# Optimization experiments

Measured on AMD Instinct MI355X. Metric: run time of the kernel, lower is better.

## Reference

```python
import jax, jax.numpy as jnp
import numpy as np
from jax import lax

K = 3           # dynamic-filter kernel size
NUM_TYPES = 216 # Qstr*Qcohe*Qangle = 3*3*24
C = 64          # in/out channels
GROUP = 4


def _conv(x, w, groups=1):
    return lax.conv_general_dilated(
        x, w, window_strides=(1, 1), padding='SAME',
        dimension_numbers=('NCHW', 'OIHW', 'NCHW'),
        feature_group_count=groups)


def setup_inputs() -> dict:
    key = jax.random.key(0)
    ks = jax.random.split(key, 7)
    B, H, W = 1, 64, 64
    x = jax.random.normal(ks[0], (B, C, H, W), dtype=jnp.float32)
    buckets = jax.random.randint(ks[1], (B, H, W), 0, NUM_TYPES)
    # body1: grouped 3x3 conv (in=out=64, groups=4 -> in/group=16)
    w1 = jax.random.normal(ks[2], (C, C // GROUP, 3, 3), dtype=jnp.float32) * 0.05
    b1 = jax.random.normal(ks[3], (C,), dtype=jnp.float32) * 0.05
    # filter embedding: one flattened (out, in*K*K + bias) filter per bucket type
    emb = jax.random.normal(ks[4], (NUM_TYPES, C * (C * K * K + 1)), dtype=jnp.float32) * 0.1
    # body2: 1x1 conv
    w2 = jax.random.normal(ks[5], (C, C, 1, 1), dtype=jnp.float32) * 0.05
    b2 = jax.random.normal(ks[6], (C,), dtype=jnp.float32) * 0.05
    return {'x': x, 'buckets': buckets, 'w1': w1, 'b1': b1, 'emb': emb, 'w2': w2, 'b2': b2}


def reference(x, buckets, w1, b1, emb, w2, b2):
    B, Cin, H, W = x.shape
    Cout = w2.shape[0]
    ckk = emb.shape[1] // Cout - 1  # in*K*K
    # body1: grouped conv + ReLU
    h = jax.nn.relu(_conv(x, w1, groups=GROUP) + b1[None, :, None, None])
    # per-pixel bucket-indexed dynamic conv
    patches = lax.conv_general_dilated_patches(
        h, (K, K), (1, 1), 'SAME',
        dimension_numbers=('NCHW', 'OIHW', 'NCHW'))  # [B, Cin*K*K, H, W]
    f = emb[buckets].reshape(B, H, W, Cout, ckk + 1)   # gathered per-pixel filters
    out = jnp.einsum('bchw,bhwoc->bohw', patches, f[..., :-1])
    out = out + jnp.transpose(f[..., -1], (0, 3, 1, 2))  # per-pixel bias
    # body2: ReLU -> 1x1 conv
    out = _conv(jax.nn.relu(out), w2) + b2[None, :, None, None]
    # residual + ReLU
    return jax.nn.relu(out + x)
```

## Files before the change

kernel.cpp:

```cpp
#include <hip/hip_runtime.h>

#define NTYPES 216
#define NPIX   4096
#define KD     576
#define ROWLEN 577
#define NPC    32
#define PSTR   640
#define MAXB   160

typedef __attribute__((ext_vector_type(8))) short short8;
typedef __attribute__((ext_vector_type(4))) float f32x4;
typedef __attribute__((ext_vector_type(4), aligned(4))) float f32x4u;
typedef __attribute__((ext_vector_type(8))) unsigned short u16x8;
typedef __attribute__((ext_vector_type(4))) unsigned short u16x4;
typedef __attribute__((ext_vector_type(2))) unsigned short u16x2;

static __device__ __forceinline__ unsigned short f2bf(float f) {
    unsigned u = __builtin_bit_cast(unsigned, f);
    unsigned r = (u + 0x7FFFu + ((u >> 16) & 1u)) >> 16;
    return (unsigned short)r;
}

__global__ __launch_bounds__(256) void prep_kernel(
        const float* __restrict__ x, const float* __restrict__ w1,
        const float* __restrict__ b1, unsigned short* __restrict__ hbf) {
    int tid = threadIdx.x;
    int flat = blockIdx.x * 256 + tid;
    int x4 = flat & 15;
    int y  = (flat >> 4) & 63;
    int c  = flat >> 10;
    int g  = c >> 4;
    const float* wrow = w1 + c * 144;
    float o0, o1, o2, o3;
    o0 = o1 = o2 = o3 = b1[c];
    #pragma unroll
    for (int ci = 0; ci < 16; ++ci) {
        const float* xp = x + (g * 16 + ci) * 4096;
        #pragma unroll
        for (int dy = 0; dy < 3; ++dy) {
            int yy = y + dy - 1;
            if (yy < 0 || yy > 63) continue;
            const float* row = xp + yy * 64 + x4 * 4;
            f32x4 mm = *(const f32x4*)row;
            float xl = (x4 > 0)  ? row[-1] : 0.f;
            float xr = (x4 < 15) ? row[4]  : 0.f;
            float wa = wrow[ci * 9 + dy * 3 + 0];
            float wb = wrow[ci * 9 + dy * 3 + 1];
            float wc = wrow[ci * 9 + dy * 3 + 2];
            o0 = fmaf(wa, xl,    fmaf(wb, mm[0], fmaf(wc, mm[1], o0)));
            o1 = fmaf(wa, mm[0], fmaf(wb, mm[1], fmaf(wc, mm[2], o1)));
            o2 = fmaf(wa, mm[1], fmaf(wb, mm[2], fmaf(wc, mm[3], o2)));
            o3 = fmaf(wa, mm[2], fmaf(wb, mm[3], fmaf(wc, xr,    o3)));
        }
    }
    int pix0 = y * 64 + x4 * 4;
    hbf[(pix0 + 0) * 64 + c] = f2bf(fmaxf(o0, 0.f));
    hbf[(pix0 + 1) * 64 + c] = f2bf(fmaxf(o1, 0.f));
    hbf[(pix0 + 2) * 64 + c] = f2bf(fmaxf(o2, 0.f));
    hbf[(pix0 + 3) * 64 + c] = f2bf(fmaxf(o3, 0.f));
}

__global__ __launch_bounds__(1024) void dyn_kernel(
        const unsigned short* __restrict__ hbf, const float* __restrict__ emb,
        const float* __restrict__ w2, const float* __restrict__ b2,
        const float* __restrict__ x, const int* __restrict__ buckets,
        float* __restrict__ out) {

    __shared__ alignas(16) unsigned short Wl[64 * PSTR];
    __shared__ alignas(16) unsigned short Pl[NPC * PSTR];
    __shared__ alignas(16) unsigned short Dl[NPC * 72];
    __shared__ alignas(16) unsigned short w2l[64 * 72];
    __shared__ float bias_l[64];
    __shared__ int pixs[MAXB];
    __shared__ int cnt_l;

    int b   = blockIdx.x;
    int tid = threadIdx.x;

    if (tid == 0) cnt_l = 0;
    __syncthreads();
    {
        int i0 = tid * 4;
        int4 v = *(const int4*)&buckets[i0];
        if (v.x == b) { int p = atomicAdd(&cnt_l, 1); if (p < MAXB) pixs[p] = i0 + 0; }
        if (v.y == b) { int p = atomicAdd(&cnt_l, 1); if (p < MAXB) pixs[p] = i0 + 1; }
        if (v.z == b) { int p = atomicAdd(&cnt_l, 1); if (p < MAXB) pixs[p] = i0 + 2; }
        if (v.w == b) { int p = atomicAdd(&cnt_l, 1); if (p < MAXB) pixs[p] = i0 + 3; }
    }
    __syncthreads();
    int n = cnt_l < MAXB ? cnt_l : MAXB;
    if (n <= 0) return;

    int gp = tid >> 5;
    int gk = tid & 31;
    unsigned short* pdst = Pl + gp * PSTR + (gp & 7) * 8;

    int pixel0 = (gp < n) ? pixs[gp] : -1;
    u16x2 p0[9];
    {
        int py = pixel0 >> 6, px = pixel0 & 63;
        #pragma unroll
        for (int dy = 0; dy < 3; ++dy) {
            int yy = py + dy - 1;
            bool yok = (yy >= 0 && yy < 64);
            #pragma unroll
            for (int dx = 0; dx < 3; ++dx) {
                int pos = dy * 3 + dx;
                int xx = px + dx - 1;
                u16x2 v = {0, 0};
                if (pixel0 >= 0 && yok && xx >= 0 && xx < 64)
                    v = *(const u16x2*)&hbf[(yy * 64 + xx) * 64 + gk * 2];
                p0[pos] = v;
            }
        }
    }

    const float* eb = emb + (size_t)b * 36928;
    #pragma unroll
    for (int it = 0; it < 5; ++it) {
        int u = tid + it * 1024;
        if (u < 4608) {
            int r  = u / 72;
            int c0 = (u - r * 72) * 8;
            const float* src = eb + r * ROWLEN + c0;
            f32x4u a  = *(const f32x4u*)src;
            f32x4u bb = *(const f32x4u*)(src + 4);
            unsigned short* wrow = &Wl[r * PSTR + (r & 7) * 8];
            #pragma unroll
            for (int j = 0; j < 8; ++j) {
                int c = c0 + j;
                int cch = c / 9, pos = c - cch * 9;
                float val = (j < 4) ? a[j] : bb[j - 4];
                wrow[pos * 64 + cch] = f2bf(val);
            }
        }
    }
    if (tid < 64) bias_l[tid] = eb[tid * ROWLEN + KD];

    if (tid < 512) {
        int o = tid >> 3, i8 = (tid & 7) * 8;
        const float* src = w2 + o * 64 + i8;
        u16x8 v;
        #pragma unroll
        for (int j = 0; j < 8; ++j) v[j] = f2bf(src[j]);
        *(u16x8*)&w2l[o * 72 + i8] = v;
    }

    #pragma unroll
    for (int pos = 0; pos < 9; ++pos)
        *(u16x2*)(pdst + pos * 64 + gk * 2) = p0[pos];

    __syncthreads();

    int lane = tid & 63;
    int wv   = tid >> 6;
    int m    = wv & 3;
    int ph   = (wv >> 2) & 1;
    int ra   = lane & 15;
    int kg   = lane >> 4;

    int rowW = m * 16 + ra;
    const unsigned short* pA = Wl + rowW * PSTR + (rowW & 7) * 8 + kg * 8;
    int ob0 = m * 16 + kg * 4;
    float bias0 = bias_l[ob0 + 0], bias1 = bias_l[ob0 + 1];
    float bias2 = bias_l[ob0 + 2], bias3 = bias_l[ob0 + 3];
    const unsigned short* pB = Pl + (ph * 16 + ra) * PSTR + (ra & 7) * 8 + kg * 8;

    for (int base = 0; base < n; base += NPC) {
        if (base > 0) {
            int pixel = (base + gp < n) ? pixs[base + gp] : -1;
            int py = pixel >> 6, px = pixel & 63;
            #pragma unroll
            for (int dy = 0; dy < 3; ++dy) {
                int yy = py + dy - 1;
                bool yok = (yy >= 0 && yy < 64);
                #pragma unroll
                for (int dx = 0; dx < 3; ++dx) {
                    int pos = dy * 3 + dx;
                    int xx = px + dx - 1;
                    u16x2 v = {0, 0};
                    if (pixel >= 0 && yok && xx >= 0 && xx < 64)
                        v = *(const u16x2*)&hbf[(yy * 64 + xx) * 64 + gk * 2];
                    *(u16x2*)(pdst + pos * 64 + gk * 2) = v;
                }
            }
            __syncthreads();
        }

        if (wv < 8) {
            f32x4 acc = {0.f, 0.f, 0.f, 0.f};
            #pragma unroll
            for (int ck = 0; ck < 9; ++ck) {
                #pragma unroll
                for (int ks = 0; ks < 2; ++ks) {
                    u16x8 av = *(const u16x8*)(pA + ck * 64 + ks * 32);
                    u16x8 bv = *(const u16x8*)(pB + ck * 64 + ks * 32);
                    acc = __builtin_amdgcn_mfma_f32_16x16x32_bf16(
                              __builtin_bit_cast(short8, av),
                              __builtin_bit_cast(short8, bv), acc, 0, 0, 0);
                }
            }
            int pi = ph * 16 + ra;
            u16x4 dv;
            dv[0] = f2bf(fmaxf(acc[0] + bias0, 0.f));
            dv[1] = f2bf(fmaxf(acc[1] + bias1, 0.f));
            dv[2] = f2bf(fmaxf(acc[2] + bias2, 0.f));
            dv[3] = f2bf(fmaxf(acc[3] + bias3, 0.f));
            *(u16x4*)&Dl[pi * 72 + ob0] = dv;
        }
        __syncthreads();

        if (wv < 8) {
            f32x4 acc2 = {0.f, 0.f, 0.f, 0.f};
            #pragma unroll
            for (int ks = 0; ks < 2; ++ks) {
                u16x8 a2  = *(const u16x8*)&w2l[(m * 16 + ra) * 72 + ks * 32 + kg * 8];
                u16x8 b2v = *(const u16x8*)&Dl[(ph * 16 + ra) * 72 + ks * 32 + kg * 8];
                acc2 = __builtin_amdgcn_mfma_f32_16x16x32_bf16(
                           __builtin_bit_cast(short8, a2),
                           __builtin_bit_cast(short8, b2v), acc2, 0, 0, 0);
            }
            int pi = ph * 16 + ra;
            int pixel = (base + pi < n) ? pixs[base + pi] : -1;
            if (pixel >= 0) {
                #pragma unroll
                for (int j = 0; j < 4; ++j) {
                    int o = ob0 + j;
                    float v = acc2[j] + b2[o] + x[o * 4096 + pixel];
                    out[o * 4096 + pixel] = fmaxf(v, 0.f);
                }
            }
        }
    }
}

extern "C" void kernel_launch(void* const* d_in, const int* in_sizes, int n_in,
                              void* d_out, int out_size, void* d_ws, size_t ws_size,
                              hipStream_t stream) {
    const float* x       = (const float*)d_in[0];
    const int*   buckets = (const int*)d_in[1];
    const float* w1      = (const float*)d_in[2];
    const float* b1      = (const float*)d_in[3];
    const float* emb     = (const float*)d_in[4];
    const float* w2      = (const float*)d_in[5];
    const float* b2      = (const float*)d_in[6];
    float* out = (float*)d_out;

    unsigned short* hbf = (unsigned short*)d_ws;

    prep_kernel<<<256, 256, 0, stream>>>(x, w1, b1, hbf);
    dyn_kernel<<<NTYPES, 1024, 0, stream>>>(hbf, emb, w2, b2, x, buckets, out);
}
```

Baseline: 31.11 us.

## Store filter rows in native channel-major order and permute patch layout instead

The shared-memory K ordering switches from position-major to the embedding's native channel-major order. Filter rows can then be converted with packed bf16 conversion instructions and written as one contiguous 16-byte store, replacing eight scattered 2-byte stores with per-element div/mod. In exchange, the patch tile is written as scattered 2-byte stores at permuted offsets. The bias and w2 staging is also moved earlier, ahead of the patch gathers.

```diff
diff --git a/kernel.cpp b/kernel.cpp
--- a/kernel.cpp
+++ b/kernel.cpp
@@ -91,6 +91,18 @@
     int n = cnt_l < MAXB ? cnt_l : MAXB;
     if (n <= 0) return;
 
+    const float* eb = emb + (size_t)b * 36928;
+
+    if (tid < 64) bias_l[tid] = eb[tid * ROWLEN + KD];
+    if (tid < 512) {
+        int o = tid >> 3, i8 = (tid & 7) * 8;
+        const float* src = w2 + o * 64 + i8;
+        u16x8 v;
+        #pragma unroll
+        for (int j = 0; j < 8; ++j) v[j] = f2bf(src[j]);
+        *(u16x8*)&w2l[o * 72 + i8] = v;
+    }
+
     int gp = tid >> 5;
     int gk = tid & 31;
     unsigned short* pdst = Pl + gp * PSTR + (gp & 7) * 8;
@@ -115,7 +127,6 @@
         }
     }
 
-    const float* eb = emb + (size_t)b * 36928;
     #pragma unroll
     for (int it = 0; it < 5; ++it) {
         int u = tid + it * 1024;
@@ -125,30 +136,28 @@
             const float* src = eb + r * ROWLEN + c0;
             f32x4u a  = *(const f32x4u*)src;
             f32x4u bb = *(const f32x4u*)(src + 4);
-            unsigned short* wrow = &Wl[r * PSTR + (r & 7) * 8];
-            #pragma unroll
-            for (int j = 0; j < 8; ++j) {
-                int c = c0 + j;
-                int cch = c / 9, pos = c - cch * 9;
-                float val = (j < 4) ? a[j] : bb[j - 4];
-                wrow[pos * 64 + cch] = f2bf(val);
-            }
-        }
-    }
-    if (tid < 64) bias_l[tid] = eb[tid * ROWLEN + KD];
-
-    if (tid < 512) {
-        int o = tid >> 3, i8 = (tid & 7) * 8;
-        const float* src = w2 + o * 64 + i8;
-        u16x8 v;
-        #pragma unroll
-        for (int j = 0; j < 8; ++j) v[j] = f2bf(src[j]);
-        *(u16x8*)&w2l[o * 72 + i8] = v;
-    }
-
-    #pragma unroll
-    for (int pos = 0; pos < 9; ++pos)
-        *(u16x2*)(pdst + pos * 64 + gk * 2) = p0[pos];
+            unsigned pk0, pk1, pk2, pk3;
+            asm("v_cvt_pk_bf16_f32 %0, %1, %2" : "=v"(pk0) : "v"(a[0]),  "v"(a[1]));
+            asm("v_cvt_pk_bf16_f32 %0, %1, %2" : "=v"(pk1) : "v"(a[2]),  "v"(a[3]));
+            asm("v_cvt_pk_bf16_f32 %0, %1, %2" : "=v"(pk2) : "v"(bb[0]), "v"(bb[1]));
+            asm("v_cvt_pk_bf16_f32 %0, %1, %2" : "=v"(pk3) : "v"(bb[2]), "v"(bb[3]));
+            u16x8 v;
+            v[0] = (unsigned short)(pk0 & 0xFFFFu); v[1] = (unsigned short)(pk0 >> 16);
+            v[2] = (unsigned short)(pk1 & 0xFFFFu); v[3] = (unsigned short)(pk1 >> 16);
+            v[4] = (unsigned short)(pk2 & 0xFFFFu); v[5] = (unsigned short)(pk2 >> 16);
+            v[6] = (unsigned short)(pk3 & 0xFFFFu); v[7] = (unsigned short)(pk3 >> 16);
+            *(u16x8*)&Wl[r * PSTR + (r & 7) * 8 + c0] = v;
+        }
+    }
+
+    {
+        int cA = (2 * gk) * 9, cB = (2 * gk + 1) * 9;
+        #pragma unroll
+        for (int pos = 0; pos < 9; ++pos) {
+            pdst[cA + pos] = p0[pos][0];
+            pdst[cB + pos] = p0[pos][1];
+        }
+    }
 
     __syncthreads();
 
@@ -170,6 +179,7 @@
         if (base > 0) {
             int pixel = (base + gp < n) ? pixs[base + gp] : -1;
             int py = pixel >> 6, px = pixel & 63;
+            int cA = (2 * gk) * 9, cB = (2 * gk + 1) * 9;
             #pragma unroll
             for (int dy = 0; dy < 3; ++dy) {
                 int yy = py + dy - 1;
@@ -181,7 +191,8 @@
                     u16x2 v = {0, 0};
                     if (pixel >= 0 && yok && xx >= 0 && xx < 64)
                         v = *(const u16x2*)&hbf[(yy * 64 + xx) * 64 + gk * 2];
-                    *(u16x2*)(pdst + pos * 64 + gk * 2) = v;
+                    pdst[cA + pos] = v[0];
+                    pdst[cB + pos] = v[1];
                 }
             }
             __syncthreads();
```

Result: no change. 30.93 us (-0.6%).
